# Kernel tuning notes

Measured on AMD Instinct MI355X. Metric: run time of the kernel, lower is better.

## Reference

```python
import jax, jax.numpy as jnp
import numpy as np

NB_HEAD = 8
SIZE_PER_HEAD = 64
MAX_LEN = 1024
MASK_PENALTY = 1e12


def setup_inputs() -> dict:
    key = jax.random.key(0)
    ks = jax.random.split(key, 6)
    B, L, D_IN = 8, MAX_LEN, 512
    D_OUT = NB_HEAD * SIZE_PER_HEAD
    return {
        "Q_seq": jax.random.normal(ks[0], (B, L, D_IN), dtype=jnp.float32),
        "K_seq": jax.random.normal(ks[1], (B, L, D_IN), dtype=jnp.float32),
        "V_seq": jax.random.normal(ks[2], (B, L, D_IN), dtype=jnp.float32),
        "WQ": jax.random.normal(ks[3], (D_IN, D_OUT), dtype=jnp.float32) * 0.03,
        "WK": jax.random.normal(ks[4], (D_IN, D_OUT), dtype=jnp.float32) * 0.03,
        "WV": jax.random.normal(ks[5], (D_IN, D_OUT), dtype=jnp.float32) * 0.03,
    }


def reference(Q_seq, K_seq, V_seq, WQ, WK, WV):
    B, L, _ = Q_seq.shape
    H, D = NB_HEAD, SIZE_PER_HEAD
    # project and split heads: [B, L, H*D] -> [B, H, L, D]
    q = (Q_seq @ WQ).reshape(B, L, H, D).transpose(0, 2, 1, 3)
    k = (K_seq @ WK).reshape(B, L, H, D).transpose(0, 2, 1, 3)
    v = (V_seq @ WV).reshape(B, L, H, D).transpose(0, 2, 1, 3)
    scale = 1.0 / jnp.sqrt(jnp.asarray(D, dtype=q.dtype))
    scores = jnp.einsum('bhqd,bhkd->bhqk', q, k) * scale  # [B,H,L,L]
    # Mask(): eye+cumsum construction == causal mask (penalize key > query)
    causal = jnp.triu(jnp.ones((L, L), dtype=scores.dtype), k=1)
    scores = scores - causal * MASK_PENALTY
    A = jax.nn.softmax(scores, axis=-1)
    O = jnp.einsum('bhqk,bhkd->bhqd', A, v)  # [B,H,L,D]
    return O.transpose(0, 2, 1, 3).reshape(B, L, H * D)
```

## Files before the change

### kernel.cpp

```cpp
#include <hip/hip_runtime.h>

#define NH 8
#define DH 64
#define SL 1024
#define NB 8
#define DIN 512
#define DOUT 512
#define PS 72

typedef __bf16 bf16x8 __attribute__((ext_vector_type(8)));
typedef float floatx4 __attribute__((ext_vector_type(4)));
typedef unsigned short ushortx8 __attribute__((ext_vector_type(8)));

__device__ __forceinline__ unsigned short f2bf(float f) {
    unsigned int u = __builtin_bit_cast(unsigned int, f);
    u += 0x7FFFu + ((u >> 16) & 1u);
    return (unsigned short)(u >> 16);
}

__device__ __forceinline__ floatx4 mfma_bf16(bf16x8 a, bf16x8 b, floatx4 c) {
    return __builtin_amdgcn_mfma_f32_16x16x32_bf16(a, b, c, 0, 0, 0);
}

__device__ __forceinline__ void gld_lds16(const unsigned short* g, unsigned short* l) {
    __builtin_amdgcn_global_load_lds(
        (const __attribute__((address_space(1))) unsigned int*)g,
        (__attribute__((address_space(3))) unsigned int*)l, 16, 0, 0);
}

__device__ __forceinline__ unsigned int pack_bf2(float a, float b) {
    return __builtin_amdgcn_perm(__builtin_bit_cast(unsigned int, b),
                                 __builtin_bit_cast(unsigned int, a), 0x07060302u);
}

__global__ __launch_bounds__(256) void prep_kernel(const float* __restrict__ Qs,
                                                   const float* __restrict__ Ks,
                                                   const float* __restrict__ Vs,
                                                   const float* __restrict__ WQ,
                                                   const float* __restrict__ WK,
                                                   const float* __restrict__ WV,
                                                   unsigned short* __restrict__ xb,
                                                   unsigned short* __restrict__ wt) {
    __shared__ unsigned short tile[64][68];
    const int bid = blockIdx.x;
    if (bid < 6144) {
        const int x = bid & 7;
        const int j = bid >> 3;
        const int z = j >> 8;
        const int t = x * 256 + (j & 255);
        const float* X = (z == 0) ? Qs : (z == 1 ? Ks : Vs);
        const int e = t * 256 + threadIdx.x;
        const int row = e >> 6, c = e & 63;
        const float4 a = *(const float4*)(X + e * 8);
        const float4 b = *(const float4*)(X + e * 8 + 4);
        ushortx8 o;
        o[0] = f2bf(a.x); o[1] = f2bf(a.y); o[2] = f2bf(a.z); o[3] = f2bf(a.w);
        o[4] = f2bf(b.x); o[5] = f2bf(b.y); o[6] = f2bf(b.z); o[7] = f2bf(b.w);
        const int dst = (((row >> 7) * 8 + (c >> 3)) * 128 + (row & 127)) * 64 +
                        (((c & 7) ^ (row & 7)) * 8);
        *(ushortx8*)(xb + z * 8192 * DIN + dst) = o;
    } else {
        const int b2 = bid - 6144;
        const int z = b2 >> 6;
        const int r = b2 & 63;
        const float* W = (z == 0) ? WQ : (z == 1 ? WK : WV);
        const int k0 = (r >> 3) * 64, n0 = (r & 7) * 64;
        const int tn = threadIdx.x & 63, tk = threadIdx.x >> 6;
#pragma unroll
        for (int i = 0; i < 16; ++i) {
            const int kk = tk + i * 4;
            tile[tn][kk] = f2bf(W[(k0 + kk) * DOUT + n0 + tn]);
        }
        __syncthreads();
#pragma unroll
        for (int i = 0; i < 16; ++i) {
            const int nn = tk + i * 4;
            const int n = n0 + nn, k = k0 + tn;
            const int dst = (((z * 4 + (n >> 7)) * 8 + (k >> 6)) * 128 + (n & 127)) * 64 +
                            ((((k >> 3) & 7) ^ (n & 7)) * 8) + (k & 7);
            wt[dst] = tile[nn][tn];
        }
    }
}

__global__ __launch_bounds__(256) void proj_kernel(const unsigned short* __restrict__ xbt,
                                                   const unsigned short* __restrict__ wtt,
                                                   unsigned short* __restrict__ qw,
                                                   unsigned short* __restrict__ ks,
                                                   unsigned short* __restrict__ vs) {
    __shared__ __align__(16) unsigned short S[32768];
    const int z = blockIdx.y;
    const int wg = blockIdx.x;
    const int ix = wg >> 3;
    const int mblk = (wg & 7) * 8 + (ix >> 2);
    const int nblk = ix & 3;
    const int w = threadIdx.x >> 6, lane = threadIdx.x & 63;
    const int l15 = lane & 15, quad = lane >> 4;
    const int wm = w >> 1, wn = w & 1;
    const int soff = lane * 8;
    const unsigned short* Ab = xbt + z * (8192 * DIN) + mblk * 8 * 8192 + (w * 4) * 512 + soff;
    const unsigned short* Bb = wtt + (z * 4 + nblk) * 8 * 8192 + (w * 4) * 512 + soff;

    floatx4 acc[4][4];
#pragma unroll
    for (int i = 0; i < 4; ++i)
#pragma unroll
        for (int j = 0; j < 4; ++j) acc[i][j] = floatx4{0.f, 0.f, 0.f, 0.f};

    auto STAGE = [&](int buf, int kblk) {
        unsigned short* Asw = &S[buf * 16384 + (w * 4) * 512];
        unsigned short* Bsw = &S[buf * 16384 + 8192 + (w * 4) * 512];
#pragma unroll
        for (int i = 0; i < 4; ++i) {
            gld_lds16(Ab + kblk * 8192 + i * 512, Asw + i * 512);
            gld_lds16(Bb + kblk * 8192 + i * 512, Bsw + i * 512);
        }
    };

    auto COMPUTE = [&](int buf) {
        const unsigned short* Asb = &S[buf * 16384];
        const unsigned short* Bsb = &S[buf * 16384 + 8192];
#pragma unroll
        for (int ksub = 0; ksub < 2; ++ksub) {
            bf16x8 af[4], bfr[4];
#pragma unroll
            for (int mi = 0; mi < 4; ++mi) {
                const int row = wm * 64 + mi * 16 + l15;
                af[mi] = *(const bf16x8*)&Asb[row * 64 + (((quad + ksub * 4) ^ (l15 & 7)) * 8)];
            }
#pragma unroll
            for (int nt = 0; nt < 4; ++nt) {
                const int row = wn * 64 + nt * 16 + l15;
                bfr[nt] = *(const bf16x8*)&Bsb[row * 64 + (((quad + ksub * 4) ^ (l15 & 7)) * 8)];
            }
#pragma unroll
            for (int mi = 0; mi < 4; ++mi)
#pragma unroll
                for (int nt = 0; nt < 4; ++nt)
                    acc[mi][nt] = mfma_bf16(af[mi], bfr[nt], acc[mi][nt]);
        }
    };

    STAGE(0, 0);
    __syncthreads();
    for (int kblk = 0; kblk < 7; ++kblk) {
        STAGE((kblk + 1) & 1, kblk + 1);
        COMPUTE(kblk & 1);
        __syncthreads();
    }
    COMPUTE(1);

    __syncthreads();
#pragma unroll
    for (int mi = 0; mi < 4; ++mi)
#pragma unroll
        for (int nt = 0; nt < 4; ++nt)
#pragma unroll
            for (int r = 0; r < 4; ++r) {
                const int a = wm * 64 + mi * 16 + quad * 4 + r;
                const int c = wn * 64 + nt * 16 + l15;
                const int h = c >> 6, dh = c & 63;
                float v = acc[mi][nt][r];
                int lidx;
                if (z == 0) {
                    v *= 0.18033688f;
                    lidx = h * 8192 + (a >> 4) * 1024 + (dh >> 3) * 128 + (a & 15) * 8 + (dh & 7);
                } else if (z == 1) {
                    lidx = (((((h << 3) + (a >> 4)) << 1) | (dh >> 5))) * 512 +
                           (a & 15) * 32 + (dh & 31);
                } else {
                    const int s64 = ((a & 15) << 2) | ((a >> 4) & 3);
                    lidx = ((((h << 1) | (a >> 6)) << 1) | (s64 >> 5)) * 2048 +
                           dh * 32 + (s64 & 31);
                }
                S[lidx] = f2bf(v);
            }
    __syncthreads();

    const int b = mblk >> 3;
    const int li0 = (mblk & 7) * 128;
    const int tid = threadIdx.x;
    unsigned short* outp = (z == 0) ? qw : (z == 1 ? ks : vs);
#pragma unroll
    for (int j = 0; j < 8; ++j) {
        const int off = j * 2048 + tid * 8;
        const ushortx8 val = *(const ushortx8*)(S + off);
        int gidx;
        if (z == 0) {
            const int h = off >> 13, o13 = off & 8191;
            gidx = ((b * 8 + nblk * 2 + h) * 64 + (li0 >> 4) + (o13 >> 10)) * 1024 + (o13 & 1023);
        } else if (z == 1) {
            const int region = off >> 9, pos = off & 511;
            const int h = region >> 4, g = (region >> 1) & 7, d5 = region & 1;
            gidx = (((b * 8 + nblk * 2 + h) * 64 + (li0 >> 4) + g) * 2 + d5) * 512 + pos;
        } else {
            const int region = off >> 11, pos = off & 2047;
            const int h = region >> 2, l6 = (region >> 1) & 1, s5 = region & 1;
            gidx = ((b * 8 + nblk * 2 + h) * 32 + (li0 >> 5) + l6 * 2 + s5) * 2048 + pos;
        }
        *(ushortx8*)(outp + gidx) = val;
    }
}

template <bool DOMASK>
__device__ __forceinline__ void frame_step(
    int kt, int m0, int l15, int quad,
    const unsigned short* __restrict__ ksb,
    const unsigned short* __restrict__ vsb,
    unsigned short* myPs,
    bf16x8 aQA0, bf16x8 aQA1, bf16x8 aQB0, bf16x8 aQB1,
    floatx4& oA0, floatx4& oA1, floatx4& oA2, floatx4& oA3,
    floatx4& oB0, floatx4& oB1, floatx4& oB2, floatx4& oB3,
    float& lA0, float& lA1, float& lA2, float& lA3,
    float& lB0, float& lB1, float& lB2, float& lB3) {
    const floatx4 zf = {0.f, 0.f, 0.f, 0.f};
    const unsigned short* kp = ksb + (kt >> 4) * 1024;
    floatx4 sA0 = zf, sA1 = zf, sA2 = zf, sA3 = zf;
    floatx4 sB0 = zf, sB1 = zf, sB2 = zf, sB3 = zf;
    __builtin_amdgcn_s_setprio(1);
#define QK_T(T, SA, SB)                                                     \
    if (!DOMASK || (kt + T * 16 <= m0 + 31)) {                              \
        const bf16x8 k0_ = *(const bf16x8*)(kp + T * 1024);                 \
        const bf16x8 k1_ = *(const bf16x8*)(kp + T * 1024 + 512);           \
        if (!DOMASK || (kt + T * 16 <= m0 + 15))                            \
            SA = mfma_bf16(aQA1, k1_, mfma_bf16(aQA0, k0_, zf));            \
        SB = mfma_bf16(aQB1, k1_, mfma_bf16(aQB0, k0_, zf));                \
    }
    QK_T(0, sA0, sB0)
    QK_T(1, sA1, sB1)
    QK_T(2, sA2, sB2)
    QK_T(3, sA3, sB3)
#undef QK_T
    __builtin_amdgcn_s_setprio(0);
    const unsigned short* vb = vsb + (kt >> 5) * 2048;
    const bf16x8 v00 = *(const bf16x8*)(vb);
    const bf16x8 v01 = *(const bf16x8*)(vb + 512);
    const bf16x8 v02 = *(const bf16x8*)(vb + 1024);
    const bf16x8 v03 = *(const bf16x8*)(vb + 1536);
    const bf16x8 v10 = *(const bf16x8*)(vb + 2048);
    const bf16x8 v11 = *(const bf16x8*)(vb + 2560);
    const bf16x8 v12 = *(const bf16x8*)(vb + 3072);
    const bf16x8 v13 = *(const bf16x8*)(vb + 3584);
#define TAIL_R(R, LA, LB)                                                    \
    {                                                                        \
        const int rowA = m0 + quad * 4 + R;                                  \
        float pa0 = __builtin_amdgcn_exp2f(sA0[R]);                          \
        float pa1 = __builtin_amdgcn_exp2f(sA1[R]);                          \
        float pa2 = __builtin_amdgcn_exp2f(sA2[R]);                          \
        float pa3 = __builtin_amdgcn_exp2f(sA3[R]);                          \
        float pb0 = __builtin_amdgcn_exp2f(sB0[R]);                          \
        float pb1 = __builtin_amdgcn_exp2f(sB1[R]);                          \
        float pb2 = __builtin_amdgcn_exp2f(sB2[R]);                          \
        float pb3 = __builtin_amdgcn_exp2f(sB3[R]);                          \
        if (DOMASK) {                                                        \
            if (kt + l15 > rowA) pa0 = 0.f;                                  \
            if (kt + 16 + l15 > rowA) pa1 = 0.f;                             \
            if (kt + 32 + l15 > rowA) pa2 = 0.f;                             \
            if (kt + 48 + l15 > rowA) pa3 = 0.f;                             \
            if (kt + l15 > rowA + 16) pb0 = 0.f;                             \
            if (kt + 16 + l15 > rowA + 16) pb1 = 0.f;                        \
            if (kt + 32 + l15 > rowA + 16) pb2 = 0.f;                        \
            if (kt + 48 + l15 > rowA + 16) pb3 = 0.f;                        \
        }                                                                    \
        LA += (pa0 + pa1) + (pa2 + pa3);                                     \
        LB += (pb0 + pb1) + (pb2 + pb3);                                     \
        uint2 pkA, pkB;                                                      \
        pkA.x = pack_bf2(pa0, pa1);                                          \
        pkA.y = pack_bf2(pa2, pa3);                                          \
        pkB.x = pack_bf2(pb0, pb1);                                          \
        pkB.y = pack_bf2(pb2, pb3);                                          \
        *(uint2*)(myPs + (quad * 4 + R) * PS + l15 * 4) = pkA;               \
        *(uint2*)(myPs + (16 + quad * 4 + R) * PS + l15 * 4) = pkB;          \
    }
    TAIL_R(0, lA0, lB0)
    TAIL_R(1, lA1, lB1)
    TAIL_R(2, lA2, lB2)
    TAIL_R(3, lA3, lB3)
#undef TAIL_R
    __builtin_amdgcn_wave_barrier();
    const bf16x8 aPA0 = *(const bf16x8*)(myPs + l15 * PS + quad * 8);
    const bf16x8 aPA1 = *(const bf16x8*)(myPs + l15 * PS + 32 + quad * 8);
    const bf16x8 aPB0 = *(const bf16x8*)(myPs + (16 + l15) * PS + quad * 8);
    const bf16x8 aPB1 = *(const bf16x8*)(myPs + (16 + l15) * PS + 32 + quad * 8);
    __builtin_amdgcn_wave_barrier();
    __builtin_amdgcn_s_setprio(1);
    oA0 = mfma_bf16(aPA1, v10, mfma_bf16(aPA0, v00, oA0));
    oA1 = mfma_bf16(aPA1, v11, mfma_bf16(aPA0, v01, oA1));
    oA2 = mfma_bf16(aPA1, v12, mfma_bf16(aPA0, v02, oA2));
    oA3 = mfma_bf16(aPA1, v13, mfma_bf16(aPA0, v03, oA3));
    oB0 = mfma_bf16(aPB1, v10, mfma_bf16(aPB0, v00, oB0));
    oB1 = mfma_bf16(aPB1, v11, mfma_bf16(aPB0, v01, oB1));
    oB2 = mfma_bf16(aPB1, v12, mfma_bf16(aPB0, v02, oB2));
    oB3 = mfma_bf16(aPB1, v13, mfma_bf16(aPB0, v03, oB3));
    __builtin_amdgcn_s_setprio(0);
}

__global__ __launch_bounds__(256) void attn_kernel(const unsigned short* __restrict__ qw,
                                                   const unsigned short* __restrict__ ksp,
                                                   const unsigned short* __restrict__ vsp,
                                                   float* __restrict__ out) {
    __shared__ union {
        unsigned short Ps[4][32 * PS];
        float Cb[2][64][42];
    } sh;
    const int w = threadIdx.x >> 6;
    const int lane = threadIdx.x & 63;
    const int l15 = lane & 15, quad = lane >> 4;
    const int s_ = blockIdx.x;
    const int xcd = s_ & 7;
    const int idx = s_ >> 3;
    const int bh = xcd * 8 + (idx & 7);
    const int xb16 = idx >> 3;
    const int b = bh >> 3, h = bh & 7;
    const int p = (w < 2) ? xb16 : 31 - xb16;
    const int half = w & 1;
    const int m0 = p * 32;

    const unsigned short* qpA = qw + (bh * 64 + 2 * p) * 1024 + quad * 128 + l15 * 8;
    const bf16x8 aQA0 = *(const bf16x8*)qpA;
    const bf16x8 aQA1 = *(const bf16x8*)(qpA + 512);
    const bf16x8 aQB0 = *(const bf16x8*)(qpA + 1024);
    const bf16x8 aQB1 = *(const bf16x8*)(qpA + 1536);

    const unsigned short* ksb = ksp + (bh * 64) * 2 * 512 + l15 * 32 + quad * 8;
    const unsigned short* vsb = vsp + (bh * 32 * 64 + l15) * 32 + quad * 8;
    unsigned short* myPs = sh.Ps[w];

    const floatx4 zf = {0.f, 0.f, 0.f, 0.f};
    floatx4 oA0 = zf, oA1 = zf, oA2 = zf, oA3 = zf;
    floatx4 oB0 = zf, oB1 = zf, oB2 = zf, oB3 = zf;
    float lA0 = 0.f, lA1 = 0.f, lA2 = 0.f, lA3 = 0.f;
    float lB0 = 0.f, lB1 = 0.f, lB2 = 0.f, lB3 = 0.f;

    const int nf = (m0 + 95) >> 6;
    const int last = nf - 1;
    for (int j = half; j < last; j += 2)
        frame_step<false>(j * 64, m0, l15, quad, ksb, vsb, myPs,
                          aQA0, aQA1, aQB0, aQB1,
                          oA0, oA1, oA2, oA3, oB0, oB1, oB2, oB3,
                          lA0, lA1, lA2, lA3, lB0, lB1, lB2, lB3);
    if ((last & 1) == half)
        frame_step<true>(last * 64, m0, l15, quad, ksb, vsb, myPs,
                         aQA0, aQA1, aQB0, aQB1,
                         oA0, oA1, oA2, oA3, oB0, oB1, oB2, oB3,
                         lA0, lA1, lA2, lA3, lB0, lB1, lB2, lB3);

    __syncthreads();
    if (half == 1) {
        float* cb = &sh.Cb[w >> 1][lane][0];
        cb[0] = oA0[0];  cb[1] = oA0[1];  cb[2] = oA0[2];  cb[3] = oA0[3];
        cb[4] = oA1[0];  cb[5] = oA1[1];  cb[6] = oA1[2];  cb[7] = oA1[3];
        cb[8] = oA2[0];  cb[9] = oA2[1];  cb[10] = oA2[2]; cb[11] = oA2[3];
        cb[12] = oA3[0]; cb[13] = oA3[1]; cb[14] = oA3[2]; cb[15] = oA3[3];
        cb[16] = oB0[0]; cb[17] = oB0[1]; cb[18] = oB0[2]; cb[19] = oB0[3];
        cb[20] = oB1[0]; cb[21] = oB1[1]; cb[22] = oB1[2]; cb[23] = oB1[3];
        cb[24] = oB2[0]; cb[25] = oB2[1]; cb[26] = oB2[2]; cb[27] = oB2[3];
        cb[28] = oB3[0]; cb[29] = oB3[1]; cb[30] = oB3[2]; cb[31] = oB3[3];
        cb[32] = lA0; cb[33] = lA1; cb[34] = lA2; cb[35] = lA3;
        cb[36] = lB0; cb[37] = lB1; cb[38] = lB2; cb[39] = lB3;
    }
    __syncthreads();
    if (half == 0) {
        const float* cb = &sh.Cb[w >> 1][lane][0];
        oA0[0] += cb[0];  oA0[1] += cb[1];  oA0[2] += cb[2];  oA0[3] += cb[3];
        oA1[0] += cb[4];  oA1[1] += cb[5];  oA1[2] += cb[6];  oA1[3] += cb[7];
        oA2[0] += cb[8];  oA2[1] += cb[9];  oA2[2] += cb[10]; oA2[3] += cb[11];
        oA3[0] += cb[12]; oA3[1] += cb[13]; oA3[2] += cb[14]; oA3[3] += cb[15];
        oB0[0] += cb[16]; oB0[1] += cb[17]; oB0[2] += cb[18]; oB0[3] += cb[19];
        oB1[0] += cb[20]; oB1[1] += cb[21]; oB1[2] += cb[22]; oB1[3] += cb[23];
        oB2[0] += cb[24]; oB2[1] += cb[25]; oB2[2] += cb[26]; oB2[3] += cb[27];
        oB3[0] += cb[28]; oB3[1] += cb[29]; oB3[2] += cb[30]; oB3[3] += cb[31];
        lA0 += cb[32]; lA1 += cb[33]; lA2 += cb[34]; lA3 += cb[35];
        lB0 += cb[36]; lB1 += cb[37]; lB2 += cb[38]; lB3 += cb[39];
#define OUT_R(R, LA, LB)                                                      \
    {                                                                         \
        float lAr = LA, lBr = LB;                                             \
        lAr += __shfl_xor(lAr, 1); lBr += __shfl_xor(lBr, 1);                 \
        lAr += __shfl_xor(lAr, 2); lBr += __shfl_xor(lBr, 2);                 \
        lAr += __shfl_xor(lAr, 4); lBr += __shfl_xor(lBr, 4);                 \
        lAr += __shfl_xor(lAr, 8); lBr += __shfl_xor(lBr, 8);                 \
        const float invA = 1.0f / lAr;                                        \
        const float invB = 1.0f / lBr;                                        \
        const int rowA = m0 + quad * 4 + R;                                   \
        float* opA = out + (b * SL + rowA) * DOUT + h * DH + l15;             \
        float* opB = opA + 16 * DOUT;                                         \
        opA[0] = oA0[R] * invA;  opA[16] = oA1[R] * invA;                     \
        opA[32] = oA2[R] * invA; opA[48] = oA3[R] * invA;                     \
        opB[0] = oB0[R] * invB;  opB[16] = oB1[R] * invB;                     \
        opB[32] = oB2[R] * invB; opB[48] = oB3[R] * invB;                     \
    }
        OUT_R(0, lA0, lB0)
        OUT_R(1, lA1, lB1)
        OUT_R(2, lA2, lB2)
        OUT_R(3, lA3, lB3)
#undef OUT_R
    }
}

extern "C" void kernel_launch(void* const* d_in, const int* in_sizes, int n_in,
                              void* d_out, int out_size, void* d_ws, size_t ws_size,
                              hipStream_t stream) {
    const float* Qs = (const float*)d_in[0];
    const float* Ks = (const float*)d_in[1];
    const float* Vs = (const float*)d_in[2];
    const float* WQ = (const float*)d_in[3];
    const float* WK = (const float*)d_in[4];
    const float* WV = (const float*)d_in[5];
    float* out = (float*)d_out;

    unsigned short* xb = (unsigned short*)d_ws;
    unsigned short* wt = xb + 3 * 8192 * DIN;
    unsigned short* qw = wt + 3 * DIN * DOUT;
    unsigned short* ks = qw + NB * NH * SL * DH;
    unsigned short* vs = ks + NB * NH * SL * DH;

    prep_kernel<<<dim3(6336), 256, 0, stream>>>(Qs, Ks, Vs, WQ, WK, WV, xb, wt);
    proj_kernel<<<dim3(256, 3), 256, 0, stream>>>(xb, wt, qw, ks, vs);
    attn_kernel<<<dim3(1024), 256, 0, stream>>>(qw, ks, vs, out);
}
```

Before: 153.0 us.

## Widen attention query tile per wave from 32 to 64 rows

Each wave now handles 64 query rows instead of 32, so every K and V fragment loaded from memory feeds four query subtiles rather than two. The grid is halved to 512 blocks, the LDS P buffer and cross-wave combine buffer are doubled, and the causal diagonal frame skips only the blocks that are fully masked. This roughly doubles accumulator register pressure, which may lower occupancy, and gives fewer, larger blocks for load balancing.

```diff
diff --git a/kernel.cpp b/kernel.cpp
--- a/kernel.cpp
+++ b/kernel.cpp
@@ -203,35 +203,90 @@
 }
 
 template <bool DOMASK>
-__device__ __forceinline__ void frame_step(
+__device__ __forceinline__ void frame64(
     int kt, int m0, int l15, int quad,
     const unsigned short* __restrict__ ksb,
     const unsigned short* __restrict__ vsb,
     unsigned short* myPs,
-    bf16x8 aQA0, bf16x8 aQA1, bf16x8 aQB0, bf16x8 aQB1,
+    bf16x8 QA0, bf16x8 QA1, bf16x8 QB0, bf16x8 QB1,
+    bf16x8 QC0, bf16x8 QC1, bf16x8 QD0, bf16x8 QD1,
     floatx4& oA0, floatx4& oA1, floatx4& oA2, floatx4& oA3,
     floatx4& oB0, floatx4& oB1, floatx4& oB2, floatx4& oB3,
+    floatx4& oC0, floatx4& oC1, floatx4& oC2, floatx4& oC3,
+    floatx4& oD0, floatx4& oD1, floatx4& oD2, floatx4& oD3,
     float& lA0, float& lA1, float& lA2, float& lA3,
-    float& lB0, float& lB1, float& lB2, float& lB3) {
+    float& lB0, float& lB1, float& lB2, float& lB3,
+    float& lC0, float& lC1, float& lC2, float& lC3,
+    float& lD0, float& lD1, float& lD2, float& lD3) {
     const floatx4 zf = {0.f, 0.f, 0.f, 0.f};
     const unsigned short* kp = ksb + (kt >> 4) * 1024;
-    floatx4 sA0 = zf, sA1 = zf, sA2 = zf, sA3 = zf;
-    floatx4 sB0 = zf, sB1 = zf, sB2 = zf, sB3 = zf;
+    const bf16x8 k00 = *(const bf16x8*)(kp);
+    const bf16x8 k01 = *(const bf16x8*)(kp + 512);
+    const bf16x8 k10 = *(const bf16x8*)(kp + 1024);
+    const bf16x8 k11 = *(const bf16x8*)(kp + 1536);
+    const bf16x8 k20 = *(const bf16x8*)(kp + 2048);
+    const bf16x8 k21 = *(const bf16x8*)(kp + 2560);
+    const bf16x8 k30 = *(const bf16x8*)(kp + 3072);
+    const bf16x8 k31 = *(const bf16x8*)(kp + 3584);
+
+    floatx4 s0 = zf, s1 = zf, s2 = zf, s3 = zf;
+    floatx4 u0 = zf, u1 = zf, u2 = zf, u3 = zf;
     __builtin_amdgcn_s_setprio(1);
-#define QK_T(T, SA, SB)                                                     \
-    if (!DOMASK || (kt + T * 16 <= m0 + 31)) {                              \
-        const bf16x8 k0_ = *(const bf16x8*)(kp + T * 1024);                 \
-        const bf16x8 k1_ = *(const bf16x8*)(kp + T * 1024 + 512);           \
-        if (!DOMASK || (kt + T * 16 <= m0 + 15))                            \
-            SA = mfma_bf16(aQA1, k1_, mfma_bf16(aQA0, k0_, zf));            \
-        SB = mfma_bf16(aQB1, k1_, mfma_bf16(aQB0, k0_, zf));                \
-    }
-    QK_T(0, sA0, sB0)
-    QK_T(1, sA1, sB1)
-    QK_T(2, sA2, sB2)
-    QK_T(3, sA3, sB3)
-#undef QK_T
+    s0 = mfma_bf16(QA1, k01, mfma_bf16(QA0, k00, zf));
+    u0 = mfma_bf16(QB1, k01, mfma_bf16(QB0, k00, zf));
+    u1 = mfma_bf16(QB1, k11, mfma_bf16(QB0, k10, zf));
+    if (!DOMASK) {
+        s1 = mfma_bf16(QA1, k11, mfma_bf16(QA0, k10, zf));
+        s2 = mfma_bf16(QA1, k21, mfma_bf16(QA0, k20, zf));
+        s3 = mfma_bf16(QA1, k31, mfma_bf16(QA0, k30, zf));
+        u2 = mfma_bf16(QB1, k21, mfma_bf16(QB0, k20, zf));
+        u3 = mfma_bf16(QB1, k31, mfma_bf16(QB0, k30, zf));
+    }
     __builtin_amdgcn_s_setprio(0);
+
+#define SMTAIL_R(R, S0, S1, S2, S3, TOFF, LACC)                              \
+    {                                                                        \
+        const int rowq = m0 + (TOFF) + quad * 4 + R;                         \
+        float p0 = __builtin_amdgcn_exp2f(S0[R]);                            \
+        float p1 = __builtin_amdgcn_exp2f(S1[R]);                            \
+        float p2 = __builtin_amdgcn_exp2f(S2[R]);                            \
+        float p3 = __builtin_amdgcn_exp2f(S3[R]);                            \
+        if (DOMASK) {                                                        \
+            if (kt + l15 > rowq) p0 = 0.f;                                   \
+            if (kt + 16 + l15 > rowq) p1 = 0.f;                              \
+            if (kt + 32 + l15 > rowq) p2 = 0.f;                              \
+            if (kt + 48 + l15 > rowq) p3 = 0.f;                              \
+        }                                                                    \
+        LACC += (p0 + p1) + (p2 + p3);                                       \
+        uint2 pk;                                                            \
+        pk.x = pack_bf2(p0, p1);                                             \
+        pk.y = pack_bf2(p2, p3);                                             \
+        *(uint2*)(myPs + ((TOFF) + quad * 4 + R) * PS + l15 * 4) = pk;       \
+    }
+    SMTAIL_R(0, s0, s1, s2, s3, 0, lA0)
+    SMTAIL_R(1, s0, s1, s2, s3, 0, lA1)
+    SMTAIL_R(2, s0, s1, s2, s3, 0, lA2)
+    SMTAIL_R(3, s0, s1, s2, s3, 0, lA3)
+    SMTAIL_R(0, u0, u1, u2, u3, 16, lB0)
+    SMTAIL_R(1, u0, u1, u2, u3, 16, lB1)
+    SMTAIL_R(2, u0, u1, u2, u3, 16, lB2)
+    SMTAIL_R(3, u0, u1, u2, u3, 16, lB3)
+
+    __builtin_amdgcn_s_setprio(1);
+    s0 = mfma_bf16(QC1, k01, mfma_bf16(QC0, k00, zf));
+    s1 = mfma_bf16(QC1, k11, mfma_bf16(QC0, k10, zf));
+    s2 = mfma_bf16(QC1, k21, mfma_bf16(QC0, k20, zf));
+    u0 = mfma_bf16(QD1, k01, mfma_bf16(QD0, k00, zf));
+    u1 = mfma_bf16(QD1, k11, mfma_bf16(QD0, k10, zf));
+    u2 = mfma_bf16(QD1, k21, mfma_bf16(QD0, k20, zf));
+    u3 = mfma_bf16(QD1, k31, mfma_bf16(QD0, k30, zf));
+    if (!DOMASK) {
+        s3 = mfma_bf16(QC1, k31, mfma_bf16(QC0, k30, zf));
+    } else {
+        s3 = zf;
+    }
+    __builtin_amdgcn_s_setprio(0);
+
     const unsigned short* vb = vsb + (kt >> 5) * 2048;
     const bf16x8 v00 = *(const bf16x8*)(vb);
     const bf16x8 v01 = *(const bf16x8*)(vb + 512);
@@ -241,57 +296,44 @@
     const bf16x8 v11 = *(const bf16x8*)(vb + 2560);
     const bf16x8 v12 = *(const bf16x8*)(vb + 3072);
     const bf16x8 v13 = *(const bf16x8*)(vb + 3584);
-#define TAIL_R(R, LA, LB)                                                    \
-    {                                                                        \
-        const int rowA = m0 + quad * 4 + R;                                  \
-        float pa0 = __builtin_amdgcn_exp2f(sA0[R]);                          \
-        float pa1 = __builtin_amdgcn_exp2f(sA1[R]);                          \
-        float pa2 = __builtin_amdgcn_exp2f(sA2[R]);                          \
-        float pa3 = __builtin_amdgcn_exp2f(sA3[R]);                          \
-        float pb0 = __builtin_amdgcn_exp2f(sB0[R]);                          \
-        float pb1 = __builtin_amdgcn_exp2f(sB1[R]);                          \
-        float pb2 = __builtin_amdgcn_exp2f(sB2[R]);                          \
-        float pb3 = __builtin_amdgcn_exp2f(sB3[R]);                          \
-        if (DOMASK) {                                                        \
-            if (kt + l15 > rowA) pa0 = 0.f;                                  \
-            if (kt + 16 + l15 > rowA) pa1 = 0.f;                             \
-            if (kt + 32 + l15 > rowA) pa2 = 0.f;                             \
-            if (kt + 48 + l15 > rowA) pa3 = 0.f;                             \
-            if (kt + l15 > rowA + 16) pb0 = 0.f;                             \
-            if (kt + 16 + l15 > rowA + 16) pb1 = 0.f;                        \
-            if (kt + 32 + l15 > rowA + 16) pb2 = 0.f;                        \
-            if (kt + 48 + l15 > rowA + 16) pb3 = 0.f;                        \
-        }                                                                    \
-        LA += (pa0 + pa1) + (pa2 + pa3);                                     \
-        LB += (pb0 + pb1) + (pb2 + pb3);                                     \
-        uint2 pkA, pkB;                                                      \
-        pkA.x = pack_bf2(pa0, pa1);                                          \
-        pkA.y = pack_bf2(pa2, pa3);                                          \
-        pkB.x = pack_bf2(pb0, pb1);                                          \
-        pkB.y = pack_bf2(pb2, pb3);                                          \
-        *(uint2*)(myPs + (quad * 4 + R) * PS + l15 * 4) = pkA;               \
-        *(uint2*)(myPs + (16 + quad * 4 + R) * PS + l15 * 4) = pkB;          \
-    }
-    TAIL_R(0, lA0, lB0)
-    TAIL_R(1, lA1, lB1)
-    TAIL_R(2, lA2, lB2)
-    TAIL_R(3, lA3, lB3)
-#undef TAIL_R
+
+    SMTAIL_R(0, s0, s1, s2, s3, 32, lC0)
+    SMTAIL_R(1, s0, s1, s2, s3, 32, lC1)
+    SMTAIL_R(2, s0, s1, s2, s3, 32, lC2)
+    SMTAIL_R(3, s0, s1, s2, s3, 32, lC3)
+    SMTAIL_R(0, u0, u1, u2, u3, 48, lD0)
+    SMTAIL_R(1, u0, u1, u2, u3, 48, lD1)
+    SMTAIL_R(2, u0, u1, u2, u3, 48, lD2)
+    SMTAIL_R(3, u0, u1, u2, u3, 48, lD3)
+#undef SMTAIL_R
+
     __builtin_amdgcn_wave_barrier();
-    const bf16x8 aPA0 = *(const bf16x8*)(myPs + l15 * PS + quad * 8);
-    const bf16x8 aPA1 = *(const bf16x8*)(myPs + l15 * PS + 32 + quad * 8);
-    const bf16x8 aPB0 = *(const bf16x8*)(myPs + (16 + l15) * PS + quad * 8);
-    const bf16x8 aPB1 = *(const bf16x8*)(myPs + (16 + l15) * PS + 32 + quad * 8);
+    const bf16x8 PA0 = *(const bf16x8*)(myPs + l15 * PS + quad * 8);
+    const bf16x8 PA1 = *(const bf16x8*)(myPs + l15 * PS + 32 + quad * 8);
+    const bf16x8 PB0 = *(const bf16x8*)(myPs + (16 + l15) * PS + quad * 8);
+    const bf16x8 PB1 = *(const bf16x8*)(myPs + (16 + l15) * PS + 32 + quad * 8);
+    const bf16x8 PC0 = *(const bf16x8*)(myPs + (32 + l15) * PS + quad * 8);
+    const bf16x8 PC1 = *(const bf16x8*)(myPs + (32 + l15) * PS + 32 + quad * 8);
+    const bf16x8 PD0 = *(const bf16x8*)(myPs + (48 + l15) * PS + quad * 8);
+    const bf16x8 PD1 = *(const bf16x8*)(myPs + (48 + l15) * PS + 32 + quad * 8);
     __builtin_amdgcn_wave_barrier();
     __builtin_amdgcn_s_setprio(1);
-    oA0 = mfma_bf16(aPA1, v10, mfma_bf16(aPA0, v00, oA0));
-    oA1 = mfma_bf16(aPA1, v11, mfma_bf16(aPA0, v01, oA1));
-    oA2 = mfma_bf16(aPA1, v12, mfma_bf16(aPA0, v02, oA2));
-    oA3 = mfma_bf16(aPA1, v13, mfma_bf16(aPA0, v03, oA3));
-    oB0 = mfma_bf16(aPB1, v10, mfma_bf16(aPB0, v00, oB0));
-    oB1 = mfma_bf16(aPB1, v11, mfma_bf16(aPB0, v01, oB1));
-    oB2 = mfma_bf16(aPB1, v12, mfma_bf16(aPB0, v02, oB2));
-    oB3 = mfma_bf16(aPB1, v13, mfma_bf16(aPB0, v03, oB3));
+    oA0 = mfma_bf16(PA1, v10, mfma_bf16(PA0, v00, oA0));
+    oA1 = mfma_bf16(PA1, v11, mfma_bf16(PA0, v01, oA1));
+    oA2 = mfma_bf16(PA1, v12, mfma_bf16(PA0, v02, oA2));
+    oA3 = mfma_bf16(PA1, v13, mfma_bf16(PA0, v03, oA3));
+    oB0 = mfma_bf16(PB1, v10, mfma_bf16(PB0, v00, oB0));
+    oB1 = mfma_bf16(PB1, v11, mfma_bf16(PB0, v01, oB1));
+    oB2 = mfma_bf16(PB1, v12, mfma_bf16(PB0, v02, oB2));
+    oB3 = mfma_bf16(PB1, v13, mfma_bf16(PB0, v03, oB3));
+    oC0 = mfma_bf16(PC1, v10, mfma_bf16(PC0, v00, oC0));
+    oC1 = mfma_bf16(PC1, v11, mfma_bf16(PC0, v01, oC1));
+    oC2 = mfma_bf16(PC1, v12, mfma_bf16(PC0, v02, oC2));
+    oC3 = mfma_bf16(PC1, v13, mfma_bf16(PC0, v03, oC3));
+    oD0 = mfma_bf16(PD1, v10, mfma_bf16(PD0, v00, oD0));
+    oD1 = mfma_bf16(PD1, v11, mfma_bf16(PD0, v01, oD1));
+    oD2 = mfma_bf16(PD1, v12, mfma_bf16(PD0, v02, oD2));
+    oD3 = mfma_bf16(PD1, v13, mfma_bf16(PD0, v03, oD3));
     __builtin_amdgcn_s_setprio(0);
 }
 
@@ -300,8 +342,8 @@
                                                    const unsigned short* __restrict__ vsp,
                                                    float* __restrict__ out) {
     __shared__ union {
-        unsigned short Ps[4][32 * PS];
-        float Cb[2][64][42];
+        unsigned short Ps[4][64 * PS];
+        float Cb[2][64][84];
     } sh;
     const int w = threadIdx.x >> 6;
     const int lane = threadIdx.x & 63;
@@ -310,17 +352,21 @@
     const int xcd = s_ & 7;
     const int idx = s_ >> 3;
     const int bh = xcd * 8 + (idx & 7);
-    const int xb16 = idx >> 3;
+    const int g8 = idx >> 3;
     const int b = bh >> 3, h = bh & 7;
-    const int p = (w < 2) ? xb16 : 31 - xb16;
+    const int gp = (w < 2) ? g8 : 15 - g8;
     const int half = w & 1;
-    const int m0 = p * 32;
-
-    const unsigned short* qpA = qw + (bh * 64 + 2 * p) * 1024 + quad * 128 + l15 * 8;
-    const bf16x8 aQA0 = *(const bf16x8*)qpA;
-    const bf16x8 aQA1 = *(const bf16x8*)(qpA + 512);
-    const bf16x8 aQB0 = *(const bf16x8*)(qpA + 1024);
-    const bf16x8 aQB1 = *(const bf16x8*)(qpA + 1536);
+    const int m0 = gp * 64;
+
+    const unsigned short* qp = qw + (bh * 64 + 4 * gp) * 1024 + quad * 128 + l15 * 8;
+    const bf16x8 QA0 = *(const bf16x8*)qp;
+    const bf16x8 QA1 = *(const bf16x8*)(qp + 512);
+    const bf16x8 QB0 = *(const bf16x8*)(qp + 1024);
+    const bf16x8 QB1 = *(const bf16x8*)(qp + 1536);
+    const bf16x8 QC0 = *(const bf16x8*)(qp + 2048);
+    const bf16x8 QC1 = *(const bf16x8*)(qp + 2560);
+    const bf16x8 QD0 = *(const bf16x8*)(qp + 3072);
+    const bf16x8 QD1 = *(const bf16x8*)(qp + 3584);
 
     const unsigned short* ksb = ksp + (bh * 64) * 2 * 512 + l15 * 32 + quad * 8;
     const unsigned short* vsb = vsp + (bh * 32 * 64 + l15) * 32 + quad * 8;
@@ -329,71 +375,86 @@
     const floatx4 zf = {0.f, 0.f, 0.f, 0.f};
     floatx4 oA0 = zf, oA1 = zf, oA2 = zf, oA3 = zf;
     floatx4 oB0 = zf, oB1 = zf, oB2 = zf, oB3 = zf;
+    floatx4 oC0 = zf, oC1 = zf, oC2 = zf, oC3 = zf;
+    floatx4 oD0 = zf, oD1 = zf, oD2 = zf, oD3 = zf;
     float lA0 = 0.f, lA1 = 0.f, lA2 = 0.f, lA3 = 0.f;
     float lB0 = 0.f, lB1 = 0.f, lB2 = 0.f, lB3 = 0.f;
-
-    const int nf = (m0 + 95) >> 6;
-    const int last = nf - 1;
+    float lC0 = 0.f, lC1 = 0.f, lC2 = 0.f, lC3 = 0.f;
+    float lD0 = 0.f, lD1 = 0.f, lD2 = 0.f, lD3 = 0.f;
+
+    const int last = gp;
     for (int j = half; j < last; j += 2)
-        frame_step<false>(j * 64, m0, l15, quad, ksb, vsb, myPs,
-                          aQA0, aQA1, aQB0, aQB1,
-                          oA0, oA1, oA2, oA3, oB0, oB1, oB2, oB3,
-                          lA0, lA1, lA2, lA3, lB0, lB1, lB2, lB3);
+        frame64<false>(j * 64, m0, l15, quad, ksb, vsb, myPs,
+                       QA0, QA1, QB0, QB1, QC0, QC1, QD0, QD1,
+                       oA0, oA1, oA2, oA3, oB0, oB1, oB2, oB3,
+                       oC0, oC1, oC2, oC3, oD0, oD1, oD2, oD3,
+                       lA0, lA1, lA2, lA3, lB0, lB1, lB2, lB3,
+                       lC0, lC1, lC2, lC3, lD0, lD1, lD2, lD3);
     if ((last & 1) == half)
-        frame_step<true>(last * 64, m0, l15, quad, ksb, vsb, myPs,
-                         aQA0, aQA1, aQB0, aQB1,
-                         oA0, oA1, oA2, oA3, oB0, oB1, oB2, oB3,
-                         lA0, lA1, lA2, lA3, lB0, lB1, lB2, lB3);
+        frame64<true>(last * 64, m0, l15, quad, ksb, vsb, myPs,
+                      QA0, QA1, QB0, QB1, QC0, QC1, QD0, QD1,
+                      oA0, oA1, oA2, oA3, oB0, oB1, oB2, oB3,
+                      oC0, oC1, oC2, oC3, oD0, oD1, oD2, oD3,
+                      lA0, lA1, lA2, lA3, lB0, lB1, lB2, lB3,
+                      lC0, lC1, lC2, lC3, lD0, lD1, lD2, lD3);
 
     __syncthreads();
     if (half == 1) {
         float* cb = &sh.Cb[w >> 1][lane][0];
-        cb[0] = oA0[0];  cb[1] = oA0[1];  cb[2] = oA0[2];  cb[3] = oA0[3];
-        cb[4] = oA1[0];  cb[5] = oA1[1];  cb[6] = oA1[2];  cb[7] = oA1[3];
-        cb[8] = oA2[0];  cb[9] = oA2[1];  cb[10] = oA2[2]; cb[11] = oA2[3];
-        cb[12] = oA3[0]; cb[13] = oA3[1]; cb[14] = oA3[2]; cb[15] = oA3[3];
-        cb[16] = oB0[0]; cb[17] = oB0[1]; cb[18] = oB0[2]; cb[19] = oB0[3];
-        cb[20] = oB1[0]; cb[21] = oB1[1]; cb[22] = oB1[2]; cb[23] = oB1[3];
-        cb[24] = oB2[0]; cb[25] = oB2[1]; cb[26] = oB2[2]; cb[27] = oB2[3];
-        cb[28] = oB3[0]; cb[29] = oB3[1]; cb[30] = oB3[2]; cb[31] = oB3[3];
-        cb[32] = lA0; cb[33] = lA1; cb[34] = lA2; cb[35] = lA3;
-        cb[36] = lB0; cb[37] = lB1; cb[38] = lB2; cb[39] = lB3;
+#define ST4(BASE, O) { cb[BASE] = O[0]; cb[BASE + 1] = O[1]; cb[BASE + 2] = O[2]; cb[BASE + 3] = O[3]; }
+        ST4(0, oA0)  ST4(4, oA1)  ST4(8, oA2)  ST4(12, oA3)
+        ST4(16, oB0) ST4(20, oB1) ST4(24, oB2) ST4(28, oB3)
+        ST4(32, oC0) ST4(36, oC1) ST4(40, oC2) ST4(44, oC3)
+        ST4(48, oD0) ST4(52, oD1) ST4(56, oD2) ST4(60, oD3)
+#undef ST4
+        cb[64] = lA0; cb[65] = lA1; cb[66] = lA2; cb[67] = lA3;
+        cb[68] = lB0; cb[69] = lB1; cb[70] = lB2; cb[71] = lB3;
+        cb[72] = lC0; cb[73] = lC1; cb[74] = lC2; cb[75] = lC3;
+        cb[76] = lD0; cb[77] = lD1; cb[78] = lD2; cb[79] = lD3;
     }
     __syncthreads();
     if (half == 0) {
         const float* cb = &sh.Cb[w >> 1][lane][0];
-        oA0[0] += cb[0];  oA0[1] += cb[1];  oA0[2] += cb[2];  oA0[3] += cb[3];
-        oA1[0] += cb[4];  oA1[1] += cb[5];  oA1[2] += cb[6];  oA1[3] += cb[7];
-        oA2[0] += cb[8];  oA2[1] += cb[9];  oA2[2] += cb[10]; oA2[3] += cb[11];
-        oA3[0] += cb[12]; oA3[1] += cb[13]; oA3[2] += cb[14]; oA3[3] += cb[15];
-        oB0[0] += cb[16]; oB0[1] += cb[17]; oB0[2] += cb[18]; oB0[3] += cb[19];
-        oB1[0] += cb[20]; oB1[1] += cb[21]; oB1[2] += cb[22]; oB1[3] += cb[23];
-        oB2[0] += cb[24]; oB2[1] += cb[25]; oB2[2] += cb[26]; oB2[3] += cb[27];
-        oB3[0] += cb[28]; oB3[1] += cb[29]; oB3[2] += cb[30]; oB3[3] += cb[31];
-        lA0 += cb[32]; lA1 += cb[33]; lA2 += cb[34]; lA3 += cb[35];
-        lB0 += cb[36]; lB1 += cb[37]; lB2 += cb[38]; lB3 += cb[39];
-#define OUT_R(R, LA, LB)                                                      \
+#define AD4(BASE, O) { O[0] += cb[BASE]; O[1] += cb[BASE + 1]; O[2] += cb[BASE + 2]; O[3] += cb[BASE + 3]; }
+        AD4(0, oA0)  AD4(4, oA1)  AD4(8, oA2)  AD4(12, oA3)
+        AD4(16, oB0) AD4(20, oB1) AD4(24, oB2) AD4(28, oB3)
+        AD4(32, oC0) AD4(36, oC1) AD4(40, oC2) AD4(44, oC3)
+        AD4(48, oD0) AD4(52, oD1) AD4(56, oD2) AD4(60, oD3)
+#undef AD4
+        lA0 += cb[64]; lA1 += cb[65]; lA2 += cb[66]; lA3 += cb[67];
+        lB0 += cb[68]; lB1 += cb[69]; lB2 += cb[70]; lB3 += cb[71];
+        lC0 += cb[72]; lC1 += cb[73]; lC2 += cb[74]; lC3 += cb[75];
+        lD0 += cb[76]; lD1 += cb[77]; lD2 += cb[78]; lD3 += cb[79];
+#define OUT_TR(R, TOFF, O0, O1, O2, O3, LR)                                   \
     {                                                                         \
-        float lAr = LA, lBr = LB;                                             \
-        lAr += __shfl_xor(lAr, 1); lBr += __shfl_xor(lBr, 1);                 \
-        lAr += __shfl_xor(lAr, 2); lBr += __shfl_xor(lBr, 2);                 \
-        lAr += __shfl_xor(lAr, 4); lBr += __shfl_xor(lBr, 4);                 \
-        lAr += __shfl_xor(lAr, 8); lBr += __shfl_xor(lBr, 8);                 \
-        const float invA = 1.0f / lAr;                                        \
-        const float invB = 1.0f / lBr;                                        \
-        const int rowA = m0 + quad * 4 + R;                                   \
-        float* opA = out + (b * SL + rowA) * DOUT + h * DH + l15;             \
-        float* opB = opA + 16 * DOUT;                                         \
-        opA[0] = oA0[R] * invA;  opA[16] = oA1[R] * invA;                     \
-        opA[32] = oA2[R] * invA; opA[48] = oA3[R] * invA;                     \
-        opB[0] = oB0[R] * invB;  opB[16] = oB1[R] * invB;                     \
-        opB[32] = oB2[R] * invB; opB[48] = oB3[R] * invB;                     \
-    }
-        OUT_R(0, lA0, lB0)
-        OUT_R(1, lA1, lB1)
-        OUT_R(2, lA2, lB2)
-        OUT_R(3, lA3, lB3)
-#undef OUT_R
+        float lr = LR;                                                        \
+        lr += __shfl_xor(lr, 1);                                              \
+        lr += __shfl_xor(lr, 2);                                              \
+        lr += __shfl_xor(lr, 4);                                              \
+        lr += __shfl_xor(lr, 8);                                              \
+        const float inv = 1.0f / lr;                                          \
+        const int rowq = m0 + (TOFF) + quad * 4 + R;                          \
+        float* op = out + (b * SL + rowq) * DOUT + h * DH + l15;              \
+        op[0] = O0[R] * inv;  op[16] = O1[R] * inv;                           \
+        op[32] = O2[R] * inv; op[48] = O3[R] * inv;                           \
+    }
+        OUT_TR(0, 0, oA0, oA1, oA2, oA3, lA0)
+        OUT_TR(1, 0, oA0, oA1, oA2, oA3, lA1)
+        OUT_TR(2, 0, oA0, oA1, oA2, oA3, lA2)
+        OUT_TR(3, 0, oA0, oA1, oA2, oA3, lA3)
+        OUT_TR(0, 16, oB0, oB1, oB2, oB3, lB0)
+        OUT_TR(1, 16, oB0, oB1, oB2, oB3, lB1)
+        OUT_TR(2, 16, oB0, oB1, oB2, oB3, lB2)
+        OUT_TR(3, 16, oB0, oB1, oB2, oB3, lB3)
+        OUT_TR(0, 32, oC0, oC1, oC2, oC3, lC0)
+        OUT_TR(1, 32, oC0, oC1, oC2, oC3, lC1)
+        OUT_TR(2, 32, oC0, oC1, oC2, oC3, lC2)
+        OUT_TR(3, 32, oC0, oC1, oC2, oC3, lC3)
+        OUT_TR(0, 48, oD0, oD1, oD2, oD3, lD0)
+        OUT_TR(1, 48, oD0, oD1, oD2, oD3, lD1)
+        OUT_TR(2, 48, oD0, oD1, oD2, oD3, lD2)
+        OUT_TR(3, 48, oD0, oD1, oD2, oD3, lD3)
+#undef OUT_TR
     }
 }
 
@@ -416,5 +477,5 @@
 
     prep_kernel<<<dim3(6336), 256, 0, stream>>>(Qs, Ks, Vs, WQ, WK, WV, xb, wt);
     proj_kernel<<<dim3(256, 3), 256, 0, stream>>>(xb, wt, qw, ks, vs);
-    attn_kernel<<<dim3(1024), 256, 0, stream>>>(qw, ks, vs, out);
-}
+    attn_kernel<<<dim3(512), 256, 0, stream>>>(qw, ks, vs, out);
+}
```

Measured after the change: 155.5 us. No clear change (+1.6%).
